# Kernel tuning notes

Measured on AMD Instinct MI355X. Metric: run time of the kernel, lower is better.

Reference implementation:

```python
import jax, jax.numpy as jnp
import numpy as np
import math

B, T, H, NH, L = 8, 1024, 192, 2, 6
FFN, K, VOCAB, OUT, WIN = 768, 3, 256, 192, 4
KC = H // NH  # per-head channels


def _get_rel(emb, t):
    pad = max(t - (WIN + 1), 0)
    start = max(WIN + 1 - t, 0)
    p = jnp.pad(emb, ((pad, pad), (0, 0)))
    return p[start:start + 2 * t - 1]


def _rel_to_abs(x):
    # [b,h,l,2l-1] -> [b,h,l,l]
    b, h, l, _ = x.shape
    x = jnp.pad(x, ((0, 0), (0, 0), (0, 0), (0, 1)))
    xf = x.reshape(b, h, l * 2 * l)
    xf = jnp.pad(xf, ((0, 0), (0, 0), (0, l - 1)))
    return xf.reshape(b, h, l + 1, 2 * l - 1)[:, :, :l, l - 1:]


def _abs_to_rel(x):
    # [b,h,l,l] -> [b,h,l,2l-1]
    b, h, l, _ = x.shape
    x = jnp.pad(x, ((0, 0), (0, 0), (0, 0), (0, l - 1)))
    xf = x.reshape(b, h, l * (2 * l - 1))
    xf = jnp.pad(xf, ((0, 0), (0, 0), (l, 0)))
    return xf.reshape(b, h, l, 2 * l)[:, :, :, 1:]


def _ln(x, g, b):
    # channels-first LayerNorm over axis 1, x: [B,C,T]
    m = jnp.mean(x, 1, keepdims=True)
    v = jnp.var(x, 1, keepdims=True)
    return (x - m) * jax.lax.rsqrt(v + 1e-5) * g[:, None] + b[:, None]


def _conv1d(x, w, b):
    y = jax.lax.conv_general_dilated(x, w, (1,), 'SAME', dimension_numbers=('NCH', 'OIH', 'NCH'))
    return y + b[:, None]


def _attn(x, attn_mask, qw, qb, kw, kb, vw, vb, ow, ob, rel_k, rel_v):
    b, d, t = x.shape
    def proj(w, bb):
        y = jnp.einsum('oc,bct->bot', w, x) + bb[:, None]
        return y.reshape(b, NH, KC, t).transpose(0, 1, 3, 2)  # [b,h,t,kc]
    q, k, v = proj(qw, qb), proj(kw, kb), proj(vw, vb)
    qs = q / math.sqrt(KC)
    scores = jnp.einsum('bhtk,bhsk->bhts', qs, k)
    scores = scores + _rel_to_abs(jnp.einsum('bhtk,mk->bhtm', qs, _get_rel(rel_k, t)))
    scores = jnp.where(attn_mask == 0, -1e4, scores)
    p = jax.nn.softmax(scores, axis=-1)
    o = jnp.einsum('bhts,bhsk->bhtk', p, v)
    o = o + jnp.einsum('bhtm,mk->bhtk', _abs_to_rel(p), _get_rel(rel_v, t))
    o = o.transpose(0, 1, 3, 2).reshape(b, d, t)
    return jnp.einsum('oc,bct->bot', ow, o) + ob[:, None]


def setup_inputs():
    key = jax.random.key(0)
    ks = iter(jax.random.split(key, 40))
    def nrm(shape, scale):
        return jax.random.normal(next(ks), shape, jnp.float32) * scale
    w = 0.05
    inp = {
        'tokens': jax.random.randint(next(ks), (B, T), 0, VOCAB),
        'x_lengths': jax.random.randint(next(ks), (B,), T // 2, T + 1),
        'emb': nrm((VOCAB, H), H ** -0.5),
        'qw': nrm((L, H, H), w), 'qb': jnp.zeros((L, H)),
        'kw': nrm((L, H, H), w), 'kb': jnp.zeros((L, H)),
        'vw': nrm((L, H, H), w), 'vb': jnp.zeros((L, H)),
        'ow': nrm((L, H, H), w), 'ob': jnp.zeros((L, H)),
        'rel_k': nrm((L, 2 * WIN + 1, KC), KC ** -0.5),
        'rel_v': nrm((L, 2 * WIN + 1, KC), KC ** -0.5),
        'ln1_g': jnp.ones((L, H)), 'ln1_b': jnp.zeros((L, H)),
        'f1w': nrm((L, FFN, H, K), w), 'f1b': jnp.zeros((L, FFN)),
        'f2w': nrm((L, H, FFN, K), w), 'f2b': jnp.zeros((L, H)),
        'ln2_g': jnp.ones((L, H)), 'ln2_b': jnp.zeros((L, H)),
        'pw': nrm((2 * OUT, H), w), 'pb': jnp.zeros((2 * OUT,)),
        'eps': jax.random.normal(next(ks), (B, OUT, T), jnp.float32),
    }
    return inp


def reference(tokens, x_lengths, emb, qw, qb, kw, kb, vw, vb, ow, ob, rel_k, rel_v,
              ln1_g, ln1_b, f1w, f1b, f2w, f2b, ln2_g, ln2_b, pw, pb, eps):
    x = emb[tokens].transpose(0, 2, 1) * math.sqrt(H)  # [B,H,T]
    x_mask = (jnp.arange(T) < x_lengths[:, None]).astype(x.dtype)[:, None, :]  # [B,1,T]
    attn_mask = x_mask[:, :, None, :] * x_mask[:, :, :, None]  # [B,1,T,T]
    x = x * x_mask
    for i in range(L):
        y = _attn(x, attn_mask, qw[i], qb[i], kw[i], kb[i], vw[i], vb[i], ow[i], ob[i], rel_k[i], rel_v[i])
        x = _ln(x + y, ln1_g[i], ln1_b[i])
        y = jax.nn.relu(_conv1d(x * x_mask, f1w[i], f1b[i]))
        y = _conv1d(y * x_mask, f2w[i], f2b[i]) * x_mask
        x = _ln(x + y, ln2_g[i], ln2_b[i])
    x = x * x_mask
    stats = (jnp.einsum('oc,bct->bot', pw, x) + pb[:, None]) * x_mask
    m, logs = stats[:, :OUT], stats[:, OUT:]
    z = m + eps * jnp.exp(logs) * x_mask
    return (z, m, logs, x, x_mask)
```

## Files before the change

### kernel.cpp

```cpp
#include <hip/hip_runtime.h>
#include <math.h>

#define BN 8
#define TN 1024
#define HN 192
#define NHN 2
#define KCN 96
#define LN 6
#define FFNN 768
#define OUTN 192
#define QSTR 104
#define GSTR 200
#define M0S 12.0f

typedef short bfrag __attribute__((ext_vector_type(8)));
typedef float f32x4 __attribute__((ext_vector_type(4)));

__device__ __forceinline__ short f2bf(float f) {
    union { float f; unsigned u; } v; v.f = f;
    unsigned r = v.u + 0x7fffu + ((v.u >> 16) & 1u);
    return (short)(r >> 16);
}
__device__ __forceinline__ float bf2f(short s) {
    union { unsigned u; float f; } v;
    v.u = ((unsigned)(unsigned short)s) << 16;
    return v.f;
}
__device__ __forceinline__ int pack2(float a, float b) {
    return (int)(unsigned short)f2bf(a) | (((int)(unsigned short)f2bf(b)) << 16);
}

#define QSCALE 0.10206207261596575f

__global__ void k_cvtall(const float* __restrict__ qw, const float* __restrict__ kw,
        const float* __restrict__ vw, const float* __restrict__ qb,
        const float* __restrict__ kb, const float* __restrict__ vb,
        const float* __restrict__ ow, const float* __restrict__ pw,
        const float* __restrict__ f1w, const float* __restrict__ f2w,
        short* __restrict__ wqkv, float* __restrict__ bqkv,
        short* __restrict__ wo16, short* __restrict__ wp16,
        short* __restrict__ wf1, short* __restrict__ wf2) {
    const int N0 = LN * 576 * 192;
    const int N1 = LN * 576;
    const int N2 = LN * HN * HN;
    const int N3 = 2 * OUTN * HN;
    const int N4 = LN * FFNN * HN * 3;
    int i = blockIdx.x * 256 + threadIdx.x;
    if (i < N0) {
        int c = i % 192, r = (i / 192) % 576, l = i / (192 * 576);
        float val, sc = 1.f;
        if (r < 192) { val = qw[((size_t)l * 192 + r) * 192 + c]; sc = QSCALE; }
        else if (r < 384) val = kw[((size_t)l * 192 + (r - 192)) * 192 + c];
        else val = vw[((size_t)l * 192 + (r - 384)) * 192 + c];
        wqkv[i] = f2bf(val * sc);
        return;
    }
    i -= N0;
    if (i < N1) {
        int r = i % 576, l = i / 576;
        bqkv[i] = (r < 192) ? qb[l * 192 + r] * QSCALE
                : (r < 384) ? kb[l * 192 + r - 192]
                            : vb[l * 192 + r - 384];
        return;
    }
    i -= N1;
    if (i < N2) { wo16[i] = f2bf(ow[i]); return; }
    i -= N2;
    if (i < N3) { wp16[i] = f2bf(pw[i]); return; }
    i -= N3;
    if (i < N4) {
        int tap = i % 3, c = (i / 3) % HN, m = (i / (3 * HN)) % FFNN, l = i / (3 * HN * FFNN);
        wf1[(((size_t)l * 3 + tap) * FFNN + m) * HN + c] = f2bf(f1w[i]);
        return;
    }
    i -= N4;
    if (i < N4) {
        int tap = i % 3, c = (i / 3) % FFNN, m = (i / (3 * FFNN)) % HN, l = i / (3 * FFNN * HN);
        wf2[(((size_t)l * 3 + tap) * HN + m) * FFNN + c] = f2bf(f2w[i]);
    }
}

__global__ __launch_bounds__(256) void k_embed(const int* __restrict__ tok,
        const int* __restrict__ lens, const float* __restrict__ emb,
        float* __restrict__ x, short* __restrict__ xb) {
    __shared__ float s[HN][65];
    const int b = blockIdx.y, t0 = blockIdx.x * 64, tid = threadIdx.x;
    const int len = lens[b];
    for (int idx = tid; idx < 64 * HN; idx += 256) {
        int tt = idx / HN, c = idx % HN;
        int t = t0 + tt;
        float v = 0.f;
        if (t < len) v = emb[tok[b * TN + t] * HN + c] * 13.856406460551018f;
        s[c][tt] = v;
    }
    __syncthreads();
    for (int idx = tid; idx < 64 * HN; idx += 256) {
        int c = idx >> 6, tt = idx & 63;
        x[((size_t)b * HN + c) * TN + t0 + tt] = s[c][tt];
    }
    for (int idx = tid; idx < 64 * 96; idx += 256) {
        int tt = idx / 96, p = idx % 96;
        ((int*)xb)[((size_t)(b * TN + t0 + tt)) * 96 + p] = pack2(s[2 * p][tt], s[2 * p + 1][tt]);
    }
}

template <bool MERGE, bool MASK_OUT>
__global__ __launch_bounds__(256) void k_g192(
        const short* __restrict__ W, const short* __restrict__ X,
        const float* __restrict__ bias, float* __restrict__ Y,
        const short* __restrict__ accP, const float* __restrict__ lPp,
        const int* __restrict__ lens, int M) {
    __shared__ short Wt[64 * GSTR];
    __shared__ short Xt[64 * GSTR];
    __shared__ float linv[128];
    const int b = blockIdx.z, m0 = blockIdx.y * 64, t0 = blockIdx.x * 64;
    const int len = lens[b];
    const int tid = threadIdx.x;
    const int w = tid >> 6, lane = tid & 63, col = lane & 15, quad = lane >> 4;

    if (t0 >= len) {
        if (MASK_OUT) {
            const int mbase = m0 + w * 16 + quad * 4;
#pragma unroll
            for (int st = 0; st < 4; ++st) {
                int t = t0 + st * 16 + col;
#pragma unroll
                for (int reg = 0; reg < 4; ++reg)
                    Y[((size_t)b * M + mbase + reg) * TN + t] = 0.f;
            }
        }
        return;
    }

    if (MERGE) {
        if (tid < 128) {
            int tt = tid & 63, h = tid >> 6;
            float l = 0.f;
#pragma unroll
            for (int sh = 0; sh < 4; ++sh)
                l += lPp[(((size_t)sh * BN + b) * NHN + h) * TN + t0 + tt];
            linv[tid] = (l > 0.f) ? 1.f / l : 0.f;
        }
        __syncthreads();
    }
    for (int i = tid; i < 1536; i += 256) {
        int mm = i / 24, part = i % 24;
        *(int4*)(Wt + mm * GSTR + part * 8) =
            *(const int4*)(W + ((size_t)(m0 + mm)) * 192 + part * 8);
    }
    for (int i = tid; i < 1536; i += 256) {
        int tt = i / 24, part = i % 24;
        if (!MERGE) {
            *(int4*)(Xt + tt * GSTR + part * 8) =
                *(const int4*)(X + ((size_t)(b * TN + t0 + tt)) * 192 + part * 8);
        } else {
            const size_t base = ((size_t)(b * TN + t0 + tt)) * 192 + part * 8;
            const size_t HSq = (size_t)BN * TN * HN;
            float a[8];
#pragma unroll
            for (int c = 0; c < 8; ++c) a[c] = 0.f;
#pragma unroll
            for (int sh = 0; sh < 4; ++sh) {
                int4 v = *(const int4*)(accP + sh * HSq + base);
                const short* sv = (const short*)&v;
#pragma unroll
                for (int c = 0; c < 8; ++c) a[c] += bf2f(sv[c]);
            }
            float li = linv[(part >= 12 ? 64 : 0) + tt];
            int4 o;
            int* oi = (int*)&o;
#pragma unroll
            for (int c = 0; c < 4; ++c) oi[c] = pack2(a[2 * c] * li, a[2 * c + 1] * li);
            *(int4*)(Xt + tt * GSTR + part * 8) = o;
        }
    }
    __syncthreads();

    f32x4 acc[4];
#pragma unroll
    for (int st = 0; st < 4; ++st) acc[st] = (f32x4){0.f, 0.f, 0.f, 0.f};
#pragma unroll
    for (int ks = 0; ks < 6; ++ks) {
        bfrag af = *(const bfrag*)(Wt + (w * 16 + col) * GSTR + ks * 32 + quad * 8);
#pragma unroll
        for (int st = 0; st < 4; ++st) {
            bfrag bf = *(const bfrag*)(Xt + (st * 16 + col) * GSTR + ks * 32 + quad * 8);
            acc[st] = __builtin_amdgcn_mfma_f32_16x16x32_bf16(af, bf, acc[st], 0, 0, 0);
        }
    }

    const int mbase = m0 + w * 16 + quad * 4;
    float bs[4];
#pragma unroll
    for (int reg = 0; reg < 4; ++reg) bs[reg] = bias[mbase + reg];
#pragma unroll
    for (int st = 0; st < 4; ++st) {
        int t = t0 + st * 16 + col;
        bool om = MASK_OUT && (t >= len);
#pragma unroll
        for (int reg = 0; reg < 4; ++reg) {
            float u = acc[st][reg] + bs[reg];
            if (om) u = 0.f;
            Y[((size_t)b * M + mbase + reg) * TN + t] = u;
        }
    }
}

__global__ __launch_bounds__(256) void k_qkv2(
        const short* __restrict__ W, const short* __restrict__ X,
        const float* __restrict__ bias, short* __restrict__ qo,
        short* __restrict__ ko, short* __restrict__ vo,
        const int* __restrict__ lens) {
    __shared__ short Wt[64 * GSTR];
    __shared__ short Xt[64 * GSTR];
    const int b = blockIdx.z, m0 = blockIdx.y * 64, t0 = blockIdx.x * 64;
    const int len = lens[b];
    const int tid = threadIdx.x;
    const int w = tid >> 6, lane = tid & 63, col = lane & 15, quad = lane >> 4;
    const int proj = m0 / 192;
    const int mbase = m0 + w * 16 + quad * 4;
    const int mloc = mbase - proj * 192;

    if (t0 >= len) {
        if (proj == 1) return;
#pragma unroll
        for (int st = 0; st < 4; ++st) {
            int t = t0 + st * 16 + col;
            if (proj == 0) {
                int2 z = {0, 0};
                *(int2*)(qo + ((size_t)(b * TN + t)) * 192 + mloc) = z;
            } else {
#pragma unroll
                for (int reg = 0; reg < 4; ++reg)
                    vo[((size_t)b * 192 + mloc + reg) * TN + t] = 0;
            }
        }
        return;
    }

    for (int i = tid; i < 1536; i += 256) {
        int mm = i / 24, part = i % 24;
        *(int4*)(Wt + mm * GSTR + part * 8) =
            *(const int4*)(W + ((size_t)(m0 + mm)) * 192 + part * 8);
    }
    for (int i = tid; i < 1536; i += 256) {
        int tt = i / 24, part = i % 24;
        *(int4*)(Xt + tt * GSTR + part * 8) =
            *(const int4*)(X + ((size_t)(b * TN + t0 + tt)) * 192 + part * 8);
    }
    __syncthreads();

    f32x4 acc[4];
#pragma unroll
    for (int st = 0; st < 4; ++st) acc[st] = (f32x4){0.f, 0.f, 0.f, 0.f};
#pragma unroll
    for (int ks = 0; ks < 6; ++ks) {
        bfrag af = *(const bfrag*)(Wt + (w * 16 + col) * GSTR + ks * 32 + quad * 8);
#pragma unroll
        for (int st = 0; st < 4; ++st) {
            bfrag bf = *(const bfrag*)(Xt + (st * 16 + col) * GSTR + ks * 32 + quad * 8);
            acc[st] = __builtin_amdgcn_mfma_f32_16x16x32_bf16(af, bf, acc[st], 0, 0, 0);
        }
    }

    float bs[4];
#pragma unroll
    for (int reg = 0; reg < 4; ++reg) bs[reg] = bias[mbase + reg];
#pragma unroll
    for (int st = 0; st < 4; ++st) {
        int t = t0 + st * 16 + col;
        float v[4];
#pragma unroll
        for (int reg = 0; reg < 4; ++reg) v[reg] = acc[st][reg] + bs[reg];
        if (proj < 2) {
            short* dst = (proj == 0) ? qo : ko;
            int2 pk;
            pk.x = pack2(v[0], v[1]);
            pk.y = pack2(v[2], v[3]);
            *(int2*)(dst + ((size_t)(b * TN + t)) * 192 + mloc) = pk;
        } else {
#pragma unroll
            for (int reg = 0; reg < 4; ++reg)
                vo[((size_t)b * 192 + mloc + reg) * TN + t] = f2bf(v[reg]);
        }
    }
}

template <int TAPS, int TT, bool RELU, bool MASK_OUT, int OUTK, int KSPLIT>
__global__ __launch_bounds__(256) void k_mgemm(
        const short* __restrict__ W, const short* __restrict__ X,
        const float* __restrict__ bias, void* __restrict__ Yv,
        float* __restrict__ Yv2, float* __restrict__ Yv3,
        const int* __restrict__ lens, int M, int Cin) {
    constexpr int P = (TAPS - 1) / 2;
    constexpr int NST = TT / 16;
    __shared__ short Wt[TAPS][64][72];
    __shared__ short Xt[TT + 2 * P][72];

    const int b = blockIdx.z;
    const int mtiles = gridDim.y / KSPLIT;
    const int kg = blockIdx.y / mtiles;
    const int m0 = (blockIdx.y % mtiles) * 64;
    const int t0 = blockIdx.x * TT;
    const int len = lens[b];
    const int tid = threadIdx.x;
    const int w = tid >> 6;
    const int lane = tid & 63;
    const int col = lane & 15;
    const int quad = lane >> 4;
    const int mbase = m0 + w * 16 + quad * 4;

    if (MASK_OUT && t0 >= len) {
#pragma unroll
        for (int st = 0; st < NST; ++st) {
            int t = t0 + st * 16 + col;
            if (OUTK == 0) {
                float* dst = (KSPLIT > 1) ? (kg == 0 ? (float*)Yv : (kg == 1 ? Yv2 : Yv3))
                                          : (float*)Yv;
#pragma unroll
                for (int reg = 0; reg < 4; ++reg)
                    dst[((size_t)b * M + mbase + reg) * TN + t] = 0.f;
            } else {
                int2 z = {0, 0};
                *(int2*)((short*)Yv + ((size_t)(b * TN + t)) * M + mbase) = z;
            }
        }
        return;
    }

    f32x4 acc[NST];
#pragma unroll
    for (int st = 0; st < NST; ++st) acc[st] = (f32x4){0.f, 0.f, 0.f, 0.f};

    const int cspan = Cin / KSPLIT;
    const int cbeg = kg * cspan;
    const int cend = cbeg + cspan;
    for (int c0 = cbeg; c0 < cend; c0 += 64) {
        __syncthreads();
        for (int i = tid; i < TAPS * 64 * 8; i += 256) {
            int tap = i / (64 * 8);
            int mm = (i / 8) & 63;
            int part = i & 7;
            *(int4*)(&Wt[tap][mm][part * 8]) =
                *(const int4*)(W + ((size_t)tap * M + m0 + mm) * Cin + c0 + part * 8);
        }
        for (int i = tid; i < (TT + 2 * P) * 8; i += 256) {
            int tt = i >> 3;
            int part = i & 7;
            int t = t0 + tt - P;
            int4 v = {0, 0, 0, 0};
            if (t >= 0 && t < TN)
                v = *(const int4*)(X + ((size_t)b * TN + t) * Cin + c0 + part * 8);
            *(int4*)(&Xt[tt][part * 8]) = v;
        }
        __syncthreads();
#pragma unroll
        for (int ks = 0; ks < 2; ++ks) {
#pragma unroll
            for (int tap = 0; tap < TAPS; ++tap) {
                bfrag af = *(const bfrag*)(&Wt[tap][w * 16 + col][ks * 32 + quad * 8]);
#pragma unroll
                for (int st = 0; st < NST; ++st) {
                    bfrag bf = *(const bfrag*)(&Xt[st * 16 + col + tap][ks * 32 + quad * 8]);
                    acc[st] = __builtin_amdgcn_mfma_f32_16x16x32_bf16(af, bf, acc[st], 0, 0, 0);
                }
            }
        }
    }

    float bs[4];
#pragma unroll
    for (int reg = 0; reg < 4; ++reg)
        bs[reg] = (KSPLIT > 1 && kg) ? 0.f : bias[mbase + reg];
#pragma unroll
    for (int st = 0; st < NST; ++st) {
        int t = t0 + st * 16 + col;
        bool om = MASK_OUT && (t >= len);
        float v[4];
#pragma unroll
        for (int reg = 0; reg < 4; ++reg) {
            float u = acc[st][reg] + bs[reg];
            if (RELU) u = fmaxf(u, 0.f);
            if (om) u = 0.f;
            v[reg] = u;
        }
        if (OUTK == 0) {
            float* dst = (KSPLIT > 1) ? (kg == 0 ? (float*)Yv : (kg == 1 ? Yv2 : Yv3))
                                      : (float*)Yv;
#pragma unroll
            for (int reg = 0; reg < 4; ++reg)
                dst[((size_t)b * M + mbase + reg) * TN + t] = v[reg];
        } else {
            int2 pk;
            pk.x = pack2(v[0], v[1]);
            pk.y = pack2(v[2], v[3]);
            *(int2*)((short*)Yv + ((size_t)(b * TN + t)) * M + mbase) = pk;
        }
    }
}

__global__ __launch_bounds__(512, 4) void k_attn4(
        const short* __restrict__ Q, const short* __restrict__ K,
        const short* __restrict__ V, const float* __restrict__ relk,
        const float* __restrict__ relv, short* __restrict__ accP,
        float* __restrict__ lP, const int* __restrict__ lens) {
    __shared__ short kt[64 * QSTR];
    __shared__ short vt[96 * 72];
    __shared__ short Pt[128 * 72];
    __shared__ short rbt[16 * QSTR];
    __shared__ float rels[128 * 12];
    __shared__ float sband[128 * 12];
    __shared__ float rvs[9 * 96];

    const int b = blockIdx.z;
    const int h = blockIdx.y >> 2, sh = blockIdx.y & 3;
    const int t0 = blockIdx.x * 128;
    const int len = lens[b];
    const int tid = threadIdx.x;
    const int w = tid >> 6;
    const int lane = tid & 63;
    const int col = lane & 15;
    const int quad = lane >> 4;

    if (t0 >= len) {
        if (tid < 128)
            lP[(((size_t)sh * BN + b) * NHN + h) * TN + t0 + tid] = 0.f;
        return;
    }

    const short* Qb = Q + ((size_t)b * TN + t0) * HN + h * KCN;
    const short* Kb = K + ((size_t)b * TN + sh * 256) * HN + h * KCN;
    const short* Vb = V + ((size_t)b * HN + h * KCN) * TN + sh * 256;

    bfrag qf[3];
#pragma unroll
    for (int ks = 0; ks < 3; ++ks)
        qf[ks] = *(const bfrag*)(Qb + (size_t)(w * 16 + col) * HN + ks * 32 + quad * 8);

    for (int i = tid; i < 9 * 96; i += 512) rvs[i] = relv[i];
    for (int i = tid; i < 16 * 96; i += 512) {
        int r = i / 96, c = i % 96;
        rbt[r * QSTR + c] = (r < 9) ? f2bf(relk[r * 96 + c]) : (short)0;
    }
    for (int i = tid; i < 128 * 12; i += 512) sband[i] = 0.f;
    __syncthreads();

    {
        f32x4 rc = (f32x4){0.f, 0.f, 0.f, 0.f};
#pragma unroll
        for (int ks = 0; ks < 3; ++ks) {
            bfrag bf = *(const bfrag*)(rbt + col * QSTR + ks * 32 + quad * 8);
            rc = __builtin_amdgcn_mfma_f32_16x16x32_bf16(qf[ks], bf, rc, 0, 0, 0);
        }
        if (col < 12) {
#pragma unroll
            for (int reg = 0; reg < 4; ++reg)
                rels[(w * 16 + quad * 4 + reg) * 12 + col] = rc[reg];
        }
    }

    float lsum[4];
    f32x4 accv[6];
#pragma unroll
    for (int r = 0; r < 4; ++r) lsum[r] = 0.f;
#pragma unroll
    for (int n = 0; n < 6; ++n) accv[n] = (f32x4){0.f, 0.f, 0.f, 0.f};

    const int rem = len - sh * 256;
    const int nj = (rem <= 0) ? 0 : ((rem >= 256) ? 4 : ((rem + 63) >> 6));

    for (int j = 0; j < nj; ++j) {
        const int s0g = sh * 256 + j * 64;
        __syncthreads();
        for (int i = tid; i < 768; i += 512) {
            int row = i / 12, part = i % 12;
            *(int4*)(kt + row * QSTR + part * 8) =
                *(const int4*)(Kb + ((size_t)(j * 64 + row)) * HN + part * 8);
        }
        for (int i = tid; i < 768; i += 512) {
            int c = i >> 3, part = i & 7;
            *(int4*)(vt + c * 72 + part * 8) =
                *(const int4*)(Vb + (size_t)c * TN + j * 64 + part * 8);
        }
        __syncthreads();

        f32x4 sacc[4];
#pragma unroll
        for (int st = 0; st < 4; ++st) sacc[st] = (f32x4){0.f, 0.f, 0.f, 0.f};
#pragma unroll
        for (int ks = 0; ks < 3; ++ks) {
#pragma unroll
            for (int st = 0; st < 4; ++st) {
                bfrag bf = *(const bfrag*)(kt + (st * 16 + col) * QSTR + ks * 32 + quad * 8);
                sacc[st] = __builtin_amdgcn_mfma_f32_16x16x32_bf16(qf[ks], bf, sacc[st], 0, 0, 0);
            }
        }

#pragma unroll
        for (int reg = 0; reg < 4; ++reg) {
            const int lq = w * 16 + quad * 4 + reg;
            const int qg = t0 + lq;
#pragma unroll
            for (int st = 0; st < 4; ++st) {
                int sg = s0g + st * 16 + col;
                float v = sacc[st][reg];
                int d = sg - qg + 4;
                bool inb = (d >= 0) && (d <= 8);
                if (inb) v += rels[lq * 12 + d];
                if (sg >= len) v = -1e4f;
                float p = __expf(v - M0S);
                if (inb) sband[lq * 12 + d] = p;
                lsum[reg] += p;
                Pt[lq * 72 + st * 16 + col] = f2bf(p);
            }
        }
#pragma unroll
        for (int ks = 0; ks < 2; ++ks) {
            bfrag af = *(const bfrag*)(Pt + (w * 16 + col) * 72 + ks * 32 + quad * 8);
#pragma unroll
            for (int nt = 0; nt < 6; ++nt) {
                bfrag bf = *(const bfrag*)(vt + (nt * 16 + col) * 72 + ks * 32 + quad * 8);
                accv[nt] = __builtin_amdgcn_mfma_f32_16x16x32_bf16(af, bf, accv[nt], 0, 0, 0);
            }
        }
    }

#pragma unroll
    for (int reg = 0; reg < 4; ++reg) {
        lsum[reg] += __shfl_xor(lsum[reg], 1);
        lsum[reg] += __shfl_xor(lsum[reg], 2);
        lsum[reg] += __shfl_xor(lsum[reg], 4);
        lsum[reg] += __shfl_xor(lsum[reg], 8);
    }
    __syncthreads();

    short* aout = accP + (size_t)sh * BN * TN * HN;
#pragma unroll
    for (int reg = 0; reg < 4; ++reg) {
        const int lq = w * 16 + quad * 4 + reg;
        const int qg = t0 + lq;
        float pb[9];
#pragma unroll
        for (int d = 0; d < 9; ++d)
            pb[d] = sband[lq * 12 + d];
#pragma unroll
        for (int nt = 0; nt < 6; ++nt) {
            int c = nt * 16 + col;
            float r = accv[nt][reg];
#pragma unroll
            for (int d = 0; d < 9; ++d) r += pb[d] * rvs[d * 96 + c];
            aout[((size_t)(b * TN + qg)) * HN + h * KCN + c] = f2bf(r);
        }
        if (col == 0)
            lP[(((size_t)sh * BN + b) * NHN + h) * TN + qg] = lsum[reg];
    }
}

template <int NADD>
__global__ __launch_bounds__(256) void k_ln(float* __restrict__ x,
        const float* __restrict__ y, const float* __restrict__ y2,
        const float* __restrict__ y3, const float* __restrict__ g,
        const float* __restrict__ bb, short* __restrict__ xb,
        const int* __restrict__ lens) {
    __shared__ float s[HN][33];
    __shared__ float red1[256], red2[256];
    __shared__ float mu[32], rs[32];
    const int b = blockIdx.y;
    const int t0 = blockIdx.x * 32;
    const int tid = threadIdx.x;
    const int len = lens[b];

    if (t0 >= len) {
        for (int idx = tid; idx < 32 * 96; idx += 256)
            ((int*)xb)[((size_t)(b * TN + t0 + idx / 96)) * 96 + idx % 96] = 0;
        return;
    }

    for (int idx = tid; idx < HN * 32; idx += 256) {
        int c = idx >> 5, tt = idx & 31;
        size_t gi = ((size_t)b * HN + c) * TN + t0 + tt;
        float v = x[gi] + y[gi];
        if (NADD >= 2) v += y2[gi];
        if (NADD >= 3) v += y3[gi];
        s[c][tt] = v;
    }
    __syncthreads();
    int tt = tid & 31, grp = tid >> 5;
    float sum = 0.f, sum2 = 0.f;
    for (int c = grp * 24; c < grp * 24 + 24; ++c) {
        float v = s[c][tt];
        sum += v;
        sum2 += v * v;
    }
    red1[tid] = sum;
    red2[tid] = sum2;
    __syncthreads();
    if (tid < 32) {
        float tot = 0.f, tot2 = 0.f;
#pragma unroll
        for (int gg = 0; gg < 8; ++gg) { tot += red1[gg * 32 + tid]; tot2 += red2[gg * 32 + tid]; }
        float mean = tot / (float)HN;
        float var = tot2 / (float)HN - mean * mean;
        mu[tid] = mean;
        rs[tid] = rsqrtf(var + 1e-5f);
    }
    __syncthreads();
    for (int idx = tid; idx < HN * 32; idx += 256) {
        int c = idx >> 5, t2 = idx & 31;
        float v = (s[c][t2] - mu[t2]) * rs[t2] * g[c] + bb[c];
        x[((size_t)b * HN + c) * TN + t0 + t2] = v;
    }
    for (int idx = tid; idx < 32 * 96; idx += 256) {
        int t2 = idx / 96, p = idx % 96;
        int c0 = 2 * p;
        float v0 = (s[c0][t2] - mu[t2]) * rs[t2] * g[c0] + bb[c0];
        float v1 = (s[c0 + 1][t2] - mu[t2]) * rs[t2] * g[c0 + 1] + bb[c0 + 1];
        if (t0 + t2 >= len) { v0 = 0.f; v1 = 0.f; }
        ((int*)xb)[((size_t)(b * TN + t0 + t2)) * 96 + p] = pack2(v0, v1);
    }
}

__global__ __launch_bounds__(256) void k_statsfin(
        const short* __restrict__ W, const short* __restrict__ X,
        const float* __restrict__ bias, const float* __restrict__ x,
        const float* __restrict__ eps, const int* __restrict__ lens,
        float* __restrict__ out) {
    __shared__ short Wt[64 * GSTR];
    __shared__ short Xt[64 * GSTR];
    const int b = blockIdx.z, o0 = blockIdx.y * 64, t0 = blockIdx.x * 64;
    const int len = lens[b];
    const int tid = threadIdx.x;
    const int w = tid >> 6, lane = tid & 63, col = lane & 15, quad = lane >> 4;
    const size_t S = (size_t)BN * OUTN * TN;

    if (t0 >= len) {
        for (int i = tid; i < 4096; i += 256) {
            int oo = i >> 6, tt = i & 63;
            size_t idx = ((size_t)b * OUTN + o0 + oo) * TN + t0 + tt;
            out[idx] = 0.f;
            out[S + idx] = 0.f;
            out[2 * S + idx] = 0.f;
            out[3 * S + idx] = 0.f;
        }
        if (o0 == 0 && tid < 64) out[4 * S + (size_t)b * TN + t0 + tid] = 0.f;
        return;
    }

    for (int i = tid; i < 1536; i += 256) {
        int tt = i / 24, part = i % 24;
        *(int4*)(Xt + tt * GSTR + part * 8) =
            *(const int4*)(X + ((size_t)(b * TN + t0 + tt)) * 192 + part * 8);
    }
    for (int i = tid; i < 1536; i += 256) {
        int mm = i / 24, part = i % 24;
        *(int4*)(Wt + mm * GSTR + part * 8) =
            *(const int4*)(W + ((size_t)(o0 + mm)) * 192 + part * 8);
    }
    __syncthreads();

    f32x4 am[4];
#pragma unroll
    for (int st = 0; st < 4; ++st) am[st] = (f32x4){0.f, 0.f, 0.f, 0.f};
#pragma unroll
    for (int ks = 0; ks < 6; ++ks) {
        bfrag af = *(const bfrag*)(Wt + (w * 16 + col) * GSTR + ks * 32 + quad * 8);
#pragma unroll
        for (int st = 0; st < 4; ++st) {
            bfrag bf = *(const bfrag*)(Xt + (st * 16 + col) * GSTR + ks * 32 + quad * 8);
            am[st] = __builtin_amdgcn_mfma_f32_16x16x32_bf16(af, bf, am[st], 0, 0, 0);
        }
    }
    __syncthreads();
    for (int i = tid; i < 1536; i += 256) {
        int mm = i / 24, part = i % 24;
        *(int4*)(Wt + mm * GSTR + part * 8) =
            *(const int4*)(W + ((size_t)(192 + o0 + mm)) * 192 + part * 8);
    }
    __syncthreads();

    f32x4 al[4];
#pragma unroll
    for (int st = 0; st < 4; ++st) al[st] = (f32x4){0.f, 0.f, 0.f, 0.f};
#pragma unroll
    for (int ks = 0; ks < 6; ++ks) {
        bfrag af = *(const bfrag*)(Wt + (w * 16 + col) * GSTR + ks * 32 + quad * 8);
#pragma unroll
        for (int st = 0; st < 4; ++st) {
            bfrag bf = *(const bfrag*)(Xt + (st * 16 + col) * GSTR + ks * 32 + quad * 8);
            al[st] = __builtin_amdgcn_mfma_f32_16x16x32_bf16(af, bf, al[st], 0, 0, 0);
        }
    }

    const int obase = o0 + w * 16 + quad * 4;
    float bm[4], bl[4];
#pragma unroll
    for (int reg = 0; reg < 4; ++reg) {
        bm[reg] = bias[obase + reg];
        bl[reg] = bias[192 + obase + reg];
    }
#pragma unroll
    for (int st = 0; st < 4; ++st) {
        int t = t0 + st * 16 + col;
        bool om = (t >= len);
#pragma unroll
        for (int reg = 0; reg < 4; ++reg) {
            float m = am[st][reg] + bm[reg];
            float ls = al[st][reg] + bl[reg];
            if (om) { m = 0.f; ls = 0.f; }
            size_t idx = ((size_t)b * OUTN + obase + reg) * TN + t;
            float e = eps[idx];
            out[idx] = om ? 0.f : m + e * __expf(ls);
            out[S + idx] = m;
            out[2 * S + idx] = ls;
        }
    }
    for (int i = tid; i < 4096; i += 256) {
        int oo = i >> 6, tt = i & 63;
        int t = t0 + tt;
        float mv = (t < len) ? 1.f : 0.f;
        size_t idx = ((size_t)b * OUTN + o0 + oo) * TN + t;
        out[3 * S + idx] = x[((size_t)b * HN + o0 + oo) * TN + t] * mv;
    }
    if (o0 == 0 && tid < 64)
        out[4 * S + (size_t)b * TN + t0 + tid] = (t0 + tid < len) ? 1.f : 0.f;
}

extern "C" void kernel_launch(void* const* d_in, const int* in_sizes, int n_in,
                              void* d_out, int out_size, void* d_ws, size_t ws_size,
                              hipStream_t stream) {
    const int* tok = (const int*)d_in[0];
    const int* lens = (const int*)d_in[1];
    const float* emb = (const float*)d_in[2];
    const float* qw = (const float*)d_in[3];
    const float* qb = (const float*)d_in[4];
    const float* kw = (const float*)d_in[5];
    const float* kb = (const float*)d_in[6];
    const float* vw = (const float*)d_in[7];
    const float* vb = (const float*)d_in[8];
    const float* ow = (const float*)d_in[9];
    const float* ob = (const float*)d_in[10];
    const float* relk = (const float*)d_in[11];
    const float* relv = (const float*)d_in[12];
    const float* ln1g = (const float*)d_in[13];
    const float* ln1b = (const float*)d_in[14];
    const float* f1w = (const float*)d_in[15];
    const float* f1b = (const float*)d_in[16];
    const float* f2w = (const float*)d_in[17];
    const float* f2b = (const float*)d_in[18];
    const float* ln2g = (const float*)d_in[19];
    const float* ln2b = (const float*)d_in[20];
    const float* pw = (const float*)d_in[21];
    const float* pb = (const float*)d_in[22];
    const float* eps = (const float*)d_in[23];

    const size_t BHT = (size_t)BN * HN * TN;
    float* ws = (float*)d_ws;
    float* x = ws;
    float* yf = ws + BHT;
    short* s_xb = (short*)(ws + 2 * BHT);
    short* s_ln = (short*)(ws + 2 * BHT + BHT / 2);
    short* s_q  = (short*)(ws + 3 * BHT);
    short* s_k  = (short*)(ws + 3 * BHT + BHT / 2);
    short* s_v  = (short*)(ws + 4 * BHT);
    float* p1   = ws + 3 * BHT;
    float* p2   = ws + 4 * BHT;
    short* accP = (short*)(ws + 5 * BHT);
    short* s_y1 = (short*)(ws + 5 * BHT);
    short* wqkv = (short*)(ws + 7 * BHT);
    short* wo16 = wqkv + (size_t)LN * 3 * HN * HN;
    short* wp16 = wo16 + (size_t)LN * HN * HN;
    short* wf1_16 = wp16 + (size_t)2 * OUTN * HN;
    short* wf2_16 = wf1_16 + (size_t)LN * 3 * FFNN * HN;
    float* bqkv = (float*)(wf2_16 + (size_t)LN * 3 * FFNN * HN);
    float* lP = bqkv + (size_t)LN * 576;

    {
        long total = (long)LN * 576 * 192 + LN * 576 + LN * HN * HN + 2 * OUTN * HN
                   + 2L * LN * FFNN * HN * 3;
        k_cvtall<<<dim3((unsigned)((total + 255) / 256)), 256, 0, stream>>>(
            qw, kw, vw, qb, kb, vb, ow, pw, f1w, f2w,
            wqkv, bqkv, wo16, wp16, wf1_16, wf2_16);
    }

    dim3 gemb(TN / 64, BN);
    k_embed<<<gemb, 256, 0, stream>>>(tok, lens, emb, x, s_xb);

    dim3 gqkv(TN / 64, 9, BN);
    dim3 gattn(TN / 128, NHN * 4, BN);
    dim3 goproj(TN / 64, HN / 64, BN);
    dim3 gf1(TN / 128, FFNN / 64, BN);
    dim3 gf2(TN / 128, 9, BN);
    dim3 gln(TN / 32, BN);

    for (int i = 0; i < LN; ++i) {
        const short* qkvwi = wqkv + (size_t)i * 576 * 192;
        const float* qkvbi = bqkv + (size_t)i * 576;
        const short* owi = wo16 + (size_t)i * HN * HN;
        const short* f1wi = wf1_16 + (size_t)i * 3 * FFNN * HN;
        const short* f2wi = wf2_16 + (size_t)i * 3 * FFNN * HN;
        const float* obi = ob + (size_t)i * HN;
        const float* rki = relk + (size_t)i * 9 * KCN;
        const float* rvi = relv + (size_t)i * 9 * KCN;
        const float* l1gi = ln1g + (size_t)i * HN;
        const float* l1bi = ln1b + (size_t)i * HN;
        const float* f1bi = f1b + (size_t)i * FFNN;
        const float* f2bi = f2b + (size_t)i * HN;
        const float* l2gi = ln2g + (size_t)i * HN;
        const float* l2bi = ln2b + (size_t)i * HN;

        k_qkv2<<<gqkv, 256, 0, stream>>>(qkvwi, s_xb, qkvbi, s_q, s_k, s_v, lens);
        k_attn4<<<gattn, 512, 0, stream>>>(s_q, s_k, s_v, rki, rvi, accP, lP, lens);
        k_g192<true, false><<<goproj, 256, 0, stream>>>(owi, nullptr, obi, yf, accP, lP, lens, HN);
        k_ln<1><<<gln, 256, 0, stream>>>(x, yf, nullptr, nullptr, l1gi, l1bi, s_ln, lens);
        k_mgemm<3, 128, true, true, 1, 1><<<gf1, 256, 0, stream>>>(f1wi, s_ln, f1bi, s_y1, nullptr, nullptr, lens, FFNN, HN);
        k_mgemm<3, 128, false, true, 0, 3><<<gf2, 256, 0, stream>>>(f2wi, s_y1, f2bi, yf, p1, p2, lens, HN, FFNN);
        k_ln<3><<<gln, 256, 0, stream>>>(x, yf, p1, p2, l2gi, l2bi, s_xb, lens);
    }

    dim3 gsf(TN / 64, OUTN / 64, BN);
    k_statsfin<<<gsf, 256, 0, stream>>>(wp16, s_xb, pb, x, eps, lens, (float*)d_out);
}
```

Before: 853.5 us.

## Fuse attention output projection with residual add and LayerNorm

Replaces the separate output-projection GEMM and the first LayerNorm kernel with one kernel. Each block covers all 192 output channels for 32 timesteps, so it can merge the split attention partials, run the projection, add the residual and bias, and normalise in place. This drops the fp32 yf round trip and one launch per layer. In exchange each block stages the full 192x192 weight in LDS, which uses far more shared memory and may lower occupancy. Variance is computed from the sum of squares rather than two-pass.

```diff
diff --git a/kernel.cpp b/kernel.cpp
--- a/kernel.cpp
+++ b/kernel.cpp
@@ -104,105 +104,150 @@
     }
 }
 
-template <bool MERGE, bool MASK_OUT>
-__global__ __launch_bounds__(256) void k_g192(
-        const short* __restrict__ W, const short* __restrict__ X,
-        const float* __restrict__ bias, float* __restrict__ Y,
+__global__ __launch_bounds__(256) void k_oln(
+        const short* __restrict__ W, const float* __restrict__ bias,
         const short* __restrict__ accP, const float* __restrict__ lPp,
-        const int* __restrict__ lens, int M) {
-    __shared__ short Wt[64 * GSTR];
-    __shared__ short Xt[64 * GSTR];
-    __shared__ float linv[128];
-    const int b = blockIdx.z, m0 = blockIdx.y * 64, t0 = blockIdx.x * 64;
+        float* __restrict__ x, const float* __restrict__ g,
+        const float* __restrict__ bb, short* __restrict__ xb,
+        const int* __restrict__ lens) {
+    __shared__ short Wt[192 * GSTR];
+    __shared__ short Xt[32 * GSTR];
+    __shared__ float s_out[HN][33];
+    __shared__ float linv[64];
+    __shared__ float red1[32 * 16], red2[32 * 16];
+    __shared__ float mu[32], rs[32];
+    const int b = blockIdx.y, t0 = blockIdx.x * 32;
     const int len = lens[b];
     const int tid = threadIdx.x;
     const int w = tid >> 6, lane = tid & 63, col = lane & 15, quad = lane >> 4;
 
     if (t0 >= len) {
-        if (MASK_OUT) {
-            const int mbase = m0 + w * 16 + quad * 4;
-#pragma unroll
-            for (int st = 0; st < 4; ++st) {
-                int t = t0 + st * 16 + col;
-#pragma unroll
-                for (int reg = 0; reg < 4; ++reg)
-                    Y[((size_t)b * M + mbase + reg) * TN + t] = 0.f;
-            }
-        }
+        for (int idx = tid; idx < 32 * 96; idx += 256)
+            ((int*)xb)[((size_t)(b * TN + t0 + idx / 96)) * 96 + idx % 96] = 0;
         return;
     }
 
-    if (MERGE) {
-        if (tid < 128) {
-            int tt = tid & 63, h = tid >> 6;
-            float l = 0.f;
-#pragma unroll
-            for (int sh = 0; sh < 4; ++sh)
-                l += lPp[(((size_t)sh * BN + b) * NHN + h) * TN + t0 + tt];
-            linv[tid] = (l > 0.f) ? 1.f / l : 0.f;
-        }
-        __syncthreads();
-    }
-    for (int i = tid; i < 1536; i += 256) {
+    if (tid < 64) {
+        int tt = tid & 31, h = tid >> 5;
+        float l = 0.f;
+#pragma unroll
+        for (int sh = 0; sh < 4; ++sh)
+            l += lPp[(((size_t)sh * BN + b) * NHN + h) * TN + t0 + tt];
+        linv[tid] = (l > 0.f) ? 1.f / l : 0.f;
+    }
+    for (int i = tid; i < 4608; i += 256) {
         int mm = i / 24, part = i % 24;
         *(int4*)(Wt + mm * GSTR + part * 8) =
-            *(const int4*)(W + ((size_t)(m0 + mm)) * 192 + part * 8);
-    }
-    for (int i = tid; i < 1536; i += 256) {
+            *(const int4*)(W + ((size_t)mm) * 192 + part * 8);
+    }
+    __syncthreads();
+    const size_t HSq = (size_t)BN * TN * HN;
+    for (int i = tid; i < 768; i += 256) {
         int tt = i / 24, part = i % 24;
-        if (!MERGE) {
-            *(int4*)(Xt + tt * GSTR + part * 8) =
-                *(const int4*)(X + ((size_t)(b * TN + t0 + tt)) * 192 + part * 8);
-        } else {
-            const size_t base = ((size_t)(b * TN + t0 + tt)) * 192 + part * 8;
-            const size_t HSq = (size_t)BN * TN * HN;
-            float a[8];
-#pragma unroll
-            for (int c = 0; c < 8; ++c) a[c] = 0.f;
-#pragma unroll
-            for (int sh = 0; sh < 4; ++sh) {
-                int4 v = *(const int4*)(accP + sh * HSq + base);
-                const short* sv = (const short*)&v;
-#pragma unroll
-                for (int c = 0; c < 8; ++c) a[c] += bf2f(sv[c]);
+        const size_t base = ((size_t)(b * TN + t0 + tt)) * 192 + part * 8;
+        float a[8];
+#pragma unroll
+        for (int c = 0; c < 8; ++c) a[c] = 0.f;
+#pragma unroll
+        for (int sh = 0; sh < 4; ++sh) {
+            int4 v = *(const int4*)(accP + sh * HSq + base);
+            const short* sv = (const short*)&v;
+#pragma unroll
+            for (int c = 0; c < 8; ++c) a[c] += bf2f(sv[c]);
+        }
+        float li = linv[(part >= 12 ? 32 : 0) + tt];
+        int4 o;
+        int* oi = (int*)&o;
+#pragma unroll
+        for (int c = 0; c < 4; ++c) oi[c] = pack2(a[2 * c] * li, a[2 * c + 1] * li);
+        *(int4*)(Xt + tt * GSTR + part * 8) = o;
+    }
+    __syncthreads();
+
+    f32x4 acc[3][2];
+#pragma unroll
+    for (int mf3 = 0; mf3 < 3; ++mf3)
+#pragma unroll
+        for (int st = 0; st < 2; ++st) acc[mf3][st] = (f32x4){0.f, 0.f, 0.f, 0.f};
+#pragma unroll
+    for (int ks = 0; ks < 6; ++ks) {
+        bfrag bf0 = *(const bfrag*)(Xt + (0 * 16 + col) * GSTR + ks * 32 + quad * 8);
+        bfrag bf1 = *(const bfrag*)(Xt + (1 * 16 + col) * GSTR + ks * 32 + quad * 8);
+#pragma unroll
+        for (int mf3 = 0; mf3 < 3; ++mf3) {
+            int mf = mf3 * 4 + w;
+            bfrag af = *(const bfrag*)(Wt + (mf * 16 + col) * GSTR + ks * 32 + quad * 8);
+            acc[mf3][0] = __builtin_amdgcn_mfma_f32_16x16x32_bf16(af, bf0, acc[mf3][0], 0, 0, 0);
+            acc[mf3][1] = __builtin_amdgcn_mfma_f32_16x16x32_bf16(af, bf1, acc[mf3][1], 0, 0, 0);
+        }
+    }
+
+    for (int i = tid; i < 6144; i += 256) {
+        int c = i >> 5, tt = i & 31;
+        s_out[c][tt] = x[((size_t)b * HN + c) * TN + t0 + tt];
+    }
+    __syncthreads();
+
+    float bsv[3][4];
+#pragma unroll
+    for (int mf3 = 0; mf3 < 3; ++mf3)
+#pragma unroll
+        for (int reg = 0; reg < 4; ++reg)
+            bsv[mf3][reg] = bias[(mf3 * 4 + w) * 16 + quad * 4 + reg];
+#pragma unroll
+    for (int st = 0; st < 2; ++st) {
+        float s1 = 0.f, s2 = 0.f;
+        int tcol = st * 16 + col;
+#pragma unroll
+        for (int mf3 = 0; mf3 < 3; ++mf3) {
+#pragma unroll
+            for (int reg = 0; reg < 4; ++reg) {
+                int row = (mf3 * 4 + w) * 16 + quad * 4 + reg;
+                float v = acc[mf3][st][reg] + bsv[mf3][reg] + s_out[row][tcol];
+                acc[mf3][st][reg] = v;
+                s1 += v;
+                s2 += v * v;
             }
-            float li = linv[(part >= 12 ? 64 : 0) + tt];
-            int4 o;
-            int* oi = (int*)&o;
-#pragma unroll
-            for (int c = 0; c < 4; ++c) oi[c] = pack2(a[2 * c] * li, a[2 * c + 1] * li);
-            *(int4*)(Xt + tt * GSTR + part * 8) = o;
-        }
-    }
-    __syncthreads();
-
-    f32x4 acc[4];
-#pragma unroll
-    for (int st = 0; st < 4; ++st) acc[st] = (f32x4){0.f, 0.f, 0.f, 0.f};
-#pragma unroll
-    for (int ks = 0; ks < 6; ++ks) {
-        bfrag af = *(const bfrag*)(Wt + (w * 16 + col) * GSTR + ks * 32 + quad * 8);
-#pragma unroll
-        for (int st = 0; st < 4; ++st) {
-            bfrag bf = *(const bfrag*)(Xt + (st * 16 + col) * GSTR + ks * 32 + quad * 8);
-            acc[st] = __builtin_amdgcn_mfma_f32_16x16x32_bf16(af, bf, acc[st], 0, 0, 0);
-        }
-    }
-
-    const int mbase = m0 + w * 16 + quad * 4;
-    float bs[4];
-#pragma unroll
-    for (int reg = 0; reg < 4; ++reg) bs[reg] = bias[mbase + reg];
-#pragma unroll
-    for (int st = 0; st < 4; ++st) {
-        int t = t0 + st * 16 + col;
-        bool om = MASK_OUT && (t >= len);
-#pragma unroll
-        for (int reg = 0; reg < 4; ++reg) {
-            float u = acc[st][reg] + bs[reg];
-            if (om) u = 0.f;
-            Y[((size_t)b * M + mbase + reg) * TN + t] = u;
-        }
+        }
+        red1[tcol * 16 + (w * 4 + quad)] = s1;
+        red2[tcol * 16 + (w * 4 + quad)] = s2;
+    }
+    __syncthreads();
+    if (tid < 32) {
+        float tot = 0.f, tot2 = 0.f;
+#pragma unroll
+        for (int gg = 0; gg < 16; ++gg) {
+            tot += red1[tid * 16 + gg];
+            tot2 += red2[tid * 16 + gg];
+        }
+        float mean = tot / (float)HN;
+        float var = tot2 / (float)HN - mean * mean;
+        mu[tid] = mean;
+        rs[tid] = rsqrtf(var + 1e-5f);
+    }
+    __syncthreads();
+#pragma unroll
+    for (int st = 0; st < 2; ++st) {
+        int tcol = st * 16 + col;
+#pragma unroll
+        for (int mf3 = 0; mf3 < 3; ++mf3) {
+#pragma unroll
+            for (int reg = 0; reg < 4; ++reg) {
+                int row = (mf3 * 4 + w) * 16 + quad * 4 + reg;
+                s_out[row][tcol] = (acc[mf3][st][reg] - mu[tcol]) * rs[tcol] * g[row] + bb[row];
+            }
+        }
+    }
+    __syncthreads();
+    for (int i = tid; i < 6144; i += 256) {
+        int c = i >> 5, tt = i & 31;
+        x[((size_t)b * HN + c) * TN + t0 + tt] = s_out[c][tt];
+    }
+    for (int idx = tid; idx < 32 * 96; idx += 256) {
+        int t2 = idx / 96, p = idx % 96;
+        float v0 = s_out[2 * p][t2], v1 = s_out[2 * p + 1][t2];
+        if (t0 + t2 >= len) { v0 = 0.f; v1 = 0.f; }
+        ((int*)xb)[((size_t)(b * TN + t0 + t2)) * 96 + p] = pack2(v0, v1);
     }
 }
 
@@ -787,7 +832,7 @@
 
     dim3 gqkv(TN / 64, 9, BN);
     dim3 gattn(TN / 128, NHN * 4, BN);
-    dim3 goproj(TN / 64, HN / 64, BN);
+    dim3 gol(TN / 32, BN);
     dim3 gf1(TN / 128, FFNN / 64, BN);
     dim3 gf2(TN / 128, 9, BN);
     dim3 gln(TN / 32, BN);
@@ -810,8 +855,7 @@
 
         k_qkv2<<<gqkv, 256, 0, stream>>>(qkvwi, s_xb, qkvbi, s_q, s_k, s_v, lens);
         k_attn4<<<gattn, 512, 0, stream>>>(s_q, s_k, s_v, rki, rvi, accP, lP, lens);
-        k_g192<true, false><<<goproj, 256, 0, stream>>>(owi, nullptr, obi, yf, accP, lP, lens, HN);
-        k_ln<1><<<gln, 256, 0, stream>>>(x, yf, nullptr, nullptr, l1gi, l1bi, s_ln, lens);
+        k_oln<<<gol, 256, 0, stream>>>(owi, obi, accP, lP, x, l1gi, l1bi, s_ln, lens);
         k_mgemm<3, 128, true, true, 1, 1><<<gf1, 256, 0, stream>>>(f1wi, s_ln, f1bi, s_y1, nullptr, nullptr, lens, FFNN, HN);
         k_mgemm<3, 128, false, true, 0, 3><<<gf2, 256, 0, stream>>>(f2wi, s_y1, f2bi, yf, p1, p2, lens, HN, FFNN);
         k_ln<3><<<gln, 256, 0, stream>>>(x, yf, p1, p2, l2gi, l2bi, s_xb, lens);
```

Result: no change. 847.6 us (-0.7%).
